# Optimization experiments

Measured on AMD Instinct MI355X. Metric: run time of the kernel, lower is better.

## Reference

```python
import jax, jax.numpy as jnp
import numpy as np

B, L, H, F, K, NBINS, T = 32, 512, 512, 512, 3, 256, 4096
EPS = 1e-8  # RMSNorm epsilon
PAD = (K - 1) // 2  # =1, matches both conv paddings in the torch module


def _conv1d(x, w, b):
    # x: [B, L, Cin], w: [K, Cin, Cout]
    return jax.lax.conv_general_dilated(
        x, w, window_strides=(1,), padding=[(PAD, PAD)],
        dimension_numbers=('NLC', 'LIO', 'NLC')) + b


def _rms(x, g):
    return g * x / (jnp.sqrt(jnp.mean(x * x, axis=-1, keepdims=True)) + EPS)


def _vpred(x, mask, w1, b1, g1, w2, b2, g2, wl, bl):
    h = _rms(jax.nn.relu(_conv1d(x, w1, b1)), g1)
    h = _rms(jax.nn.relu(_conv1d(h, w2, b2)), g2)
    out = (h @ wl + bl)[..., 0]  # [B, L]
    return jnp.where(mask, 0.0, out)


def _proj(x, w1, b1, w2, b2):
    return jax.nn.relu(jax.nn.relu(x @ w1 + b1) @ w2 + b2)


def _length_regulate(x, dur, max_len):
    # Vectorized equivalent of LengthRegulator: repeat phoneme i dur[b,i] times, pad to max_len.
    cum = jnp.cumsum(dur, axis=1)               # [B, L]
    mel_len = cum[:, -1]                        # [B]
    t = jnp.arange(max_len)                     # [T]
    idx = jax.vmap(lambda c: jnp.searchsorted(c, t, side='right'))(cum)  # [B, T]
    idx = jnp.minimum(idx, x.shape[1] - 1)
    out = jnp.take_along_axis(x, idx[:, :, None], axis=1)  # [B, T, H]
    valid = (t[None, :] < mel_len[:, None])
    return out * valid[:, :, None].astype(x.dtype), mel_len


def setup_inputs() -> dict:
    key = jax.random.key(0)
    ks = iter(jax.random.split(key, 64))
    n = lambda *s: jax.random.normal(next(ks), s, jnp.float32) * 0.05
    inp = {}
    inp['x'] = jax.random.normal(next(ks), (B, L, H), jnp.float32)
    inp['embedding'] = jax.random.normal(next(ks), (B, L, H), jnp.float32)
    inp['src_mask'] = jnp.zeros((B, L), bool)
    inp['duration_target'] = jax.random.randint(next(ks), (B, L), 0, 9, jnp.int32)
    inp['pitch_target'] = jax.random.normal(next(ks), (B, L), jnp.float32)
    inp['energy_target'] = jax.random.normal(next(ks), (B, L), jnp.float32)
    inp['max_len'] = T
    for p in ['dur', 'pit', 'eng']:
        inp[p + '_w1'] = n(K, H, F); inp[p + '_b1'] = jnp.zeros(F, jnp.float32)
        inp[p + '_g1'] = jnp.ones(F, jnp.float32)
        inp[p + '_w2'] = n(K, F, F); inp[p + '_b2'] = jnp.zeros(F, jnp.float32)
        inp[p + '_g2'] = jnp.ones(F, jnp.float32)
        inp[p + '_wl'] = n(F, 1); inp[p + '_bl'] = jnp.zeros(1, jnp.float32)
    for p in ['pp', 'ep', 'sp']:
        inp[p + '_w1'] = n(H, H); inp[p + '_b1'] = jnp.zeros(H, jnp.float32)
        inp[p + '_w2'] = n(H, H); inp[p + '_b2'] = jnp.zeros(H, jnp.float32)
    inp['pitch_bins'] = jnp.linspace(-3.0, 3.0, NBINS - 1)
    inp['energy_bins'] = jnp.linspace(-3.0, 3.0, NBINS - 1)
    inp['pitch_emb'] = n(NBINS, H)
    inp['energy_emb'] = n(NBINS, H)
    return inp


def reference(x, embedding, src_mask, duration_target, pitch_target, energy_target, max_len,
              dur_w1, dur_b1, dur_g1, dur_w2, dur_b2, dur_g2, dur_wl, dur_bl,
              pit_w1, pit_b1, pit_g1, pit_w2, pit_b2, pit_g2, pit_wl, pit_bl,
              eng_w1, eng_b1, eng_g1, eng_w2, eng_b2, eng_g2, eng_wl, eng_bl,
              pp_w1, pp_b1, pp_w2, pp_b2,
              ep_w1, ep_b1, ep_w2, ep_b2,
              sp_w1, sp_b1, sp_w2, sp_b2,
              pitch_bins, energy_bins, pitch_emb, energy_emb):
    log_dur = _vpred(x, src_mask, dur_w1, dur_b1, dur_g1, dur_w2, dur_b2, dur_g2, dur_wl, dur_bl)
    pit_pred = _vpred(x + _proj(embedding, pp_w1, pp_b1, pp_w2, pp_b2), src_mask,
                      pit_w1, pit_b1, pit_g1, pit_w2, pit_b2, pit_g2, pit_wl, pit_bl)
    pitch_embedding = pitch_emb[jnp.searchsorted(pitch_bins, pitch_target)]  # torch.bucketize right=False == side='left'
    eng_pred = _vpred(x + _proj(embedding, ep_w1, ep_b1, ep_w2, ep_b2), src_mask,
                      eng_w1, eng_b1, eng_g1, eng_w2, eng_b2, eng_g2, eng_wl, eng_bl)
    energy_embedding = energy_emb[jnp.searchsorted(energy_bins, energy_target)]
    xo = x + energy_embedding + pitch_embedding + _proj(embedding, sp_w1, sp_b1, sp_w2, sp_b2)
    out, mel_len = _length_regulate(xo, duration_target, max_len)
    return (out, pit_pred, eng_pred, log_dur, mel_len)
```

## Files before the change

kernel.cpp:

```cpp
#include <hip/hip_runtime.h>

#define Bv    32
#define Lv    512
#define Hv    512
#define Fv    512
#define Tv    4096
#define Mv    (Bv*Lv)
#define NBINSv 256

#define OUT_OFF 0
#define PIT_OFF (Bv*(size_t)Tv*Hv)
#define ENG_OFF (PIT_OFF + Mv)
#define DUR_OFF (ENG_OFF + Mv)
#define MEL_OFF (DUR_OFF + Mv)

typedef unsigned short ushort;
typedef __attribute__((ext_vector_type(8))) short   bf16x8;
typedef __attribute__((ext_vector_type(4))) float   f32x4;
typedef __attribute__((ext_vector_type(8))) unsigned short u16x8;

__device__ __forceinline__ float b2f(ushort u) {
    union { float f; unsigned u; } x; x.u = ((unsigned)u) << 16; return x.f;
}
__device__ __forceinline__ ushort f2b(float f) {
    union { float f; unsigned u; } x; x.f = f;
    unsigned r = x.u + 0x7fffu + ((x.u >> 16) & 1u);
    return (ushort)(r >> 16);
}

#define GLL16(g, l) __builtin_amdgcn_global_load_lds( \
    (const __attribute__((address_space(1))) void*)(g), \
    (__attribute__((address_space(3))) void*)(l), 16, 0, 0)

template<int NZ> struct GArgs {
    const ushort* A[NZ];
    const ushort* W[NZ];
    const float*  bias[NZ];
    ushort*       C[NZ];
};
struct RmsArgs   { const ushort* h[3]; const float* g[3]; ushort* o[3]; };
struct RlArgs    { const ushort* h[3]; const float* g[3]; const float* wl[3]; const float* bl[3]; };
struct TransArgs { const float* src[6]; ushort* dst[6]; };
struct ConvArgs  { const float* src[2]; ushort* dst[2]; };

template<int NTAPS, int EPI, int NZ>
__global__ __launch_bounds__(256) void gemm_bf16_kernel(
    GArgs<NZ> ga, const float* __restrict__ res, const float* __restrict__ pe,
    const float* __restrict__ ee, const int* __restrict__ idxp,
    const int* __restrict__ idxe, const ushort* __restrict__ zp)
{
    constexpr int KTOT = NTAPS * 512;
    const int z = (NZ > 1) ? blockIdx.z : 0;
    const ushort* __restrict__ A    = ga.A[z];
    const ushort* __restrict__ Bt   = ga.W[z];
    const float*  __restrict__ bias = ga.bias[z];
    ushort*       __restrict__ C    = ga.C[z];

    __shared__ ushort As[128 * 32];
    __shared__ ushort Bs[128 * 32];

    const int tid = threadIdx.x;
    const int n0 = blockIdx.x * 128;
    const int m0 = blockIdx.y * 128;

    const int sar = tid >> 2;
    const int sl  = tid & 3;

    const int lane = tid & 63;
    const int w    = tid >> 6;
    const int wm   = (w & 1) * 64;
    const int wn   = (w >> 1) * 64;
    const int lr   = lane & 15;
    const int q    = lane >> 4;

    f32x4 acc[4][4];
    #pragma unroll
    for (int i = 0; i < 4; ++i)
        #pragma unroll
        for (int j = 0; j < 4; ++j) {
            f32x4 zz = {0.f, 0.f, 0.f, 0.f};
            acc[i][j] = zz;
        }

    for (int kt = 0; kt < NTAPS * 16; ++kt) {
        const int tap = (NTAPS == 3) ? (kt >> 4) : 0;
        const int kin = (NTAPS == 3) ? ((kt & 15) << 5) : (kt << 5);

        #pragma unroll
        for (int r = 0; r < 2; ++r) {
            const int row = sar + r * 64;
            const int m   = m0 + row;
            const int qg  = (sl - (row >> 1)) & 3;
            const ushort* asrc;
            if (NTAPS == 3) {
                const int l  = m & (Lv - 1);
                const int ls = l + tap - 1;
                asrc = ((unsigned)ls < (unsigned)Lv)
                     ? A + (size_t)(m + tap - 1) * 512 + kin + qg * 8
                     : zp;
            } else {
                asrc = A + (size_t)m * 512 + kin + qg * 8;
            }
            GLL16(asrc, &As[row * 32 + sl * 8]);
            const ushort* bsrc = Bt + (size_t)(n0 + row) * KTOT + tap * 512 + kin + qg * 8;
            GLL16(bsrc, &Bs[row * 32 + sl * 8]);
        }
        __syncthreads();

        bf16x8 af[4], bfr[4];
        #pragma unroll
        for (int i = 0; i < 4; ++i) {
            const int rm = wm + i * 16 + lr;
            af[i]  = *(const bf16x8*)&As[rm * 32 + (((q + (rm >> 1)) & 3) << 3)];
            const int rn = wn + i * 16 + lr;
            bfr[i] = *(const bf16x8*)&Bs[rn * 32 + (((q + (rn >> 1)) & 3) << 3)];
        }
        #pragma unroll
        for (int i = 0; i < 4; ++i)
            #pragma unroll
            for (int j = 0; j < 4; ++j)
                acc[i][j] = __builtin_amdgcn_mfma_f32_16x16x32_bf16(
                                af[i], bfr[j], acc[i][j], 0, 0, 0);
        __syncthreads();
    }

    #pragma unroll
    for (int i = 0; i < 4; ++i) {
        #pragma unroll
        for (int r = 0; r < 4; ++r) {
            const int m = m0 + wm + i * 16 + q * 4 + r;
            const size_t ro = (size_t)m * 512;
            int ip = 0, ie = 0;
            if (EPI == 2) { ip = idxp[m]; ie = idxe[m]; }
            #pragma unroll
            for (int j = 0; j < 4; ++j) {
                const int n = n0 + wn + j * 16 + lr;
                float v = acc[i][j][r] + bias[n];
                v = fmaxf(v, 0.f);
                if (EPI >= 1) v += res[ro + n];
                if (EPI == 2) v += pe[(size_t)ip * 512 + n] + ee[(size_t)ie * 512 + n];
                C[ro + n] = f2b(v);
            }
        }
    }
}

__global__ __launch_bounds__(256) void convert_kernel(ConvArgs ca)
{
    const float* __restrict__ X  = ca.src[blockIdx.y];
    ushort*      __restrict__ Xb = ca.dst[blockIdx.y];
    const size_t i = (size_t)blockIdx.x * 256 + threadIdx.x;
    const float4 a = ((const float4*)X)[2 * i];
    const float4 b = ((const float4*)X)[2 * i + 1];
    u16x8 o;
    o[0] = f2b(a.x); o[1] = f2b(a.y); o[2] = f2b(a.z); o[3] = f2b(a.w);
    o[4] = f2b(b.x); o[5] = f2b(b.y); o[6] = f2b(b.z); o[7] = f2b(b.w);
    *(u16x8*)(Xb + i * 8) = o;
}

__global__ __launch_bounds__(256) void transpose_kernel(TransArgs ta, int Ktot)
{
    const float* __restrict__ W  = ta.src[blockIdx.z];
    ushort*      __restrict__ Wt = ta.dst[blockIdx.z];
    __shared__ float t[32][33];
    const int k0 = blockIdx.x * 32, n0 = blockIdx.y * 32;
    const int r = threadIdx.x >> 5, c = threadIdx.x & 31;
    #pragma unroll
    for (int rr = 0; rr < 4; ++rr)
        t[r + rr * 8][c] = W[(size_t)(k0 + r + rr * 8) * 512 + n0 + c];
    __syncthreads();
    #pragma unroll
    for (int rr = 0; rr < 4; ++rr)
        Wt[(size_t)(n0 + r + rr * 8) * Ktot + k0 + c] = f2b(t[c][r + rr * 8]);
}

__global__ __launch_bounds__(128) void rms_kernel(RmsArgs ra)
{
    const int z = blockIdx.y;
    const int row = blockIdx.x;
    const int tid = threadIdx.x;
    const ushort* __restrict__ h = ra.h[z];
    const ushort4 hv = ((const ushort4*)(h + (size_t)row * 512))[tid];
    const float v0 = b2f(hv.x), v1 = b2f(hv.y), v2 = b2f(hv.z), v3 = b2f(hv.w);
    float ss = v0 * v0 + v1 * v1 + v2 * v2 + v3 * v3;
    #pragma unroll
    for (int off = 32; off; off >>= 1) ss += __shfl_down(ss, off, 64);
    __shared__ float p[2];
    if ((tid & 63) == 0) p[tid >> 6] = ss;
    __syncthreads();
    const float tot = p[0] + p[1];
    const float inv = 1.f / (sqrtf(tot * (1.f / 512.f)) + 1e-8f);
    const float4 gv = ((const float4*)ra.g[z])[tid];
    ushort4 ov;
    ov.x = f2b(gv.x * v0 * inv); ov.y = f2b(gv.y * v1 * inv);
    ov.z = f2b(gv.z * v2 * inv); ov.w = f2b(gv.w * v3 * inv);
    ((ushort4*)(ra.o[z] + (size_t)row * 512))[tid] = ov;
}

__global__ __launch_bounds__(256) void rmslin_kernel(
    RlArgs ra, const unsigned char* __restrict__ mask, float* __restrict__ predbase)
{
    const int z = blockIdx.y;
    const int wave = threadIdx.x >> 6, lane = threadIdx.x & 63;
    const int row = blockIdx.x * 4 + wave;
    const ushort* __restrict__ h = ra.h[z];
    const bf16x8 hv = *(const bf16x8*)(h + (size_t)row * 512 + lane * 8);
    const float4 g0 = *(const float4*)(ra.g[z] + lane * 8);
    const float4 g1 = *(const float4*)(ra.g[z] + lane * 8 + 4);
    const float4 w0 = *(const float4*)(ra.wl[z] + lane * 8);
    const float4 w1 = *(const float4*)(ra.wl[z] + lane * 8 + 4);
    float hf[8];
    #pragma unroll
    for (int t = 0; t < 8; ++t) hf[t] = b2f((ushort)hv[t]);
    float ss = 0.f, sgw = 0.f;
    #pragma unroll
    for (int t = 0; t < 8; ++t) ss += hf[t] * hf[t];
    sgw += hf[0]*g0.x*w0.x + hf[1]*g0.y*w0.y + hf[2]*g0.z*w0.z + hf[3]*g0.w*w0.w;
    sgw += hf[4]*g1.x*w1.x + hf[5]*g1.y*w1.y + hf[6]*g1.z*w1.z + hf[7]*g1.w*w1.w;
    #pragma unroll
    for (int off = 32; off; off >>= 1) {
        ss  += __shfl_down(ss,  off, 64);
        sgw += __shfl_down(sgw, off, 64);
    }
    if (lane == 0) {
        const float inv = 1.f / (sqrtf(ss * (1.f / 512.f)) + 1e-8f);
        predbase[(size_t)z * Mv + row] = mask[row] ? 0.f : (sgw * inv + ra.bl[z][0]);
    }
}

__global__ __launch_bounds__(256) void idx_kernel(
    const float* __restrict__ pt, const float* __restrict__ et,
    const float* __restrict__ pbins, const float* __restrict__ ebins,
    int* __restrict__ idxp, int* __restrict__ idxe)
{
    __shared__ float pb[NBINSv - 1], ebn[NBINSv - 1];
    const int tid = threadIdx.x;
    if (tid < NBINSv - 1) { pb[tid] = pbins[tid]; ebn[tid] = ebins[tid]; }
    __syncthreads();
    const int m = blockIdx.x * 256 + tid;
    const float pv = pt[m], ev = et[m];
    int lo = 0, hi = NBINSv - 1;
    while (lo < hi) { int mid = (lo + hi) >> 1; if (pb[mid] < pv) lo = mid + 1; else hi = mid; }
    idxp[m] = lo;
    lo = 0; hi = NBINSv - 1;
    while (lo < hi) { int mid = (lo + hi) >> 1; if (ebn[mid] < ev) lo = mid + 1; else hi = mid; }
    idxe[m] = lo;
}

__global__ __launch_bounds__(512) void cumsum_kernel(
    const int* __restrict__ dur, int* __restrict__ cum,
    int* __restrict__ melint, float* __restrict__ melout)
{
    __shared__ int s[Lv];
    const int b = blockIdx.x, tid = threadIdx.x;
    s[tid] = dur[b * Lv + tid];
    __syncthreads();
    for (int off = 1; off < Lv; off <<= 1) {
        int t = (tid >= off) ? s[tid - off] : 0;
        __syncthreads();
        s[tid] += t;
        __syncthreads();
    }
    cum[b * Lv + tid] = s[tid];
    if (tid == Lv - 1) { melint[b] = s[tid]; melout[b] = (float)s[tid]; }
}

__global__ __launch_bounds__(256) void tmap_kernel(
    const int* __restrict__ cum, const int* __restrict__ melint,
    int* __restrict__ tmap)
{
    const int bt = blockIdx.x * 256 + threadIdx.x;
    const int b = bt >> 12;
    const int t = bt & (Tv - 1);
    const int* c = cum + b * Lv;
    int lo = 0, hi = Lv;
    while (lo < hi) { int mid = (lo + hi) >> 1; if (c[mid] <= t) lo = mid + 1; else hi = mid; }
    tmap[bt] = (t < melint[b]) ? (b * Lv + min(lo, Lv - 1)) : -1;
}

__global__ __launch_bounds__(128) void regulate_kernel(
    const ushort* __restrict__ xo, const int* __restrict__ tmap,
    float* __restrict__ out)
{
    const int bt = blockIdx.x;
    const int src = tmap[bt];
    float4 v = make_float4(0.f, 0.f, 0.f, 0.f);
    if (src >= 0) {
        const ushort4 u = ((const ushort4*)(xo + (size_t)src * 512))[threadIdx.x];
        v.x = b2f(u.x); v.y = b2f(u.y); v.z = b2f(u.z); v.w = b2f(u.w);
    }
    ((float4*)(out + (size_t)bt * 512))[threadIdx.x] = v;
}

extern "C" void kernel_launch(void* const* d_in, const int* in_sizes, int n_in,
                              void* d_out, int out_size, void* d_ws, size_t ws_size,
                              hipStream_t stream)
{
    const float* x    = (const float*)d_in[0];
    const float* emb  = (const float*)d_in[1];
    const unsigned char* mask = (const unsigned char*)d_in[2];
    const int*   durt = (const int*)d_in[3];
    const float* pt   = (const float*)d_in[4];
    const float* et   = (const float*)d_in[5];
    const float* dw1 = (const float*)d_in[7],  *db1 = (const float*)d_in[8],
               * dg1 = (const float*)d_in[9],  *dw2 = (const float*)d_in[10],
               * db2 = (const float*)d_in[11], *dg2 = (const float*)d_in[12],
               * dwl = (const float*)d_in[13], *dbl = (const float*)d_in[14];
    const float* pw1 = (const float*)d_in[15], *pb1 = (const float*)d_in[16],
               * pg1 = (const float*)d_in[17], *pw2 = (const float*)d_in[18],
               * pb2 = (const float*)d_in[19], *pg2 = (const float*)d_in[20],
               * pwl = (const float*)d_in[21], *pbl = (const float*)d_in[22];
    const float* ew1 = (const float*)d_in[23], *eb1 = (const float*)d_in[24],
               * eg1 = (const float*)d_in[25], *ew2 = (const float*)d_in[26],
               * eb2 = (const float*)d_in[27], *eg2 = (const float*)d_in[28],
               * ewl = (const float*)d_in[29], *ebl = (const float*)d_in[30];
    const float* ppw1 = (const float*)d_in[31], *ppb1 = (const float*)d_in[32],
               * ppw2 = (const float*)d_in[33], *ppb2 = (const float*)d_in[34];
    const float* epw1 = (const float*)d_in[35], *epb1 = (const float*)d_in[36],
               * epw2 = (const float*)d_in[37], *epb2 = (const float*)d_in[38];
    const float* spw1 = (const float*)d_in[39], *spb1 = (const float*)d_in[40],
               * spw2 = (const float*)d_in[41], *spb2 = (const float*)d_in[42];
    const float* pbins = (const float*)d_in[43];
    const float* ebins = (const float*)d_in[44];
    const float* pemb  = (const float*)d_in[45];
    const float* eemb  = (const float*)d_in[46];

    float* outf = (float*)d_out;

    int*    cum    = (int*)d_ws;
    int*    melint = cum + 16384;
    int*    idxp   = melint + 64;
    int*    idxe   = idxp + 16384;
    ushort* zp     = (ushort*)(idxe + 16384);
    int*    tmap   = idxe + 16448;
    ushort* xob    = (ushort*)((float*)d_ws + 262144);

    #define OBUF(i) ((ushort*)(outf + (size_t)(i) * 4194304))
    ushort* xb  = OBUF(0);   ushort* eb  = OBUF(1);
    ushort* pA0 = OBUF(2);   ushort* pA1 = OBUF(3);  ushort* pA2 = OBUF(4);
    ushort* xp  = OBUF(5);   ushort* xe  = OBUF(6);
    ushort* c0  = OBUF(7);   ushort* c1  = OBUF(8);  ushort* c2  = OBUF(9);
    ushort* r0  = OBUF(10);  ushort* r1  = OBUF(11); ushort* r2  = OBUF(12);
    ushort* wt[12];
    {
        size_t off = 13ull * 4194304;
        for (int i = 0; i < 6; ++i)  { wt[i] = (ushort*)(outf + off); off += 393216; }
        for (int i = 6; i < 12; ++i) { wt[i] = (ushort*)(outf + off); off += 131072; }
    }

    hipMemsetAsync(zp, 0, 64, stream);

    { ConvArgs ca = {{x, emb}, {xb, eb}};
      convert_kernel<<<dim3(4096, 2), 256, 0, stream>>>(ca); }
    { TransArgs ta = {{dw1, dw2, pw1, pw2, ew1, ew2}, {wt[0], wt[1], wt[2], wt[3], wt[4], wt[5]}};
      transpose_kernel<<<dim3(48, 16, 6), 256, 0, stream>>>(ta, 1536); }
    { TransArgs ta = {{ppw1, ppw2, epw1, epw2, spw1, spw2},
                      {wt[6], wt[7], wt[8], wt[9], wt[10], wt[11]}};
      transpose_kernel<<<dim3(16, 16, 6), 256, 0, stream>>>(ta, 512); }

    idx_kernel<<<Mv / 256, 256, 0, stream>>>(pt, et, pbins, ebins, idxp, idxe);
    cumsum_kernel<<<Bv, Lv, 0, stream>>>(durt, cum, melint, outf + MEL_OFF);
    tmap_kernel<<<Bv * Tv / 256, 256, 0, stream>>>(cum, melint, tmap);

    const dim3 g3(Fv / 128, Mv / 128, 3);
    const dim3 g2(Fv / 128, Mv / 128, 2);
    const dim3 g1(Fv / 128, Mv / 128, 1);

    { GArgs<3> a = {{eb, eb, eb}, {wt[6], wt[8], wt[10]}, {ppb1, epb1, spb1}, {pA0, pA1, pA2}};
      gemm_bf16_kernel<1, 0, 3><<<g3, 256, 0, stream>>>(a, nullptr, nullptr, nullptr,
                                                        nullptr, nullptr, zp); }
    { GArgs<2> a = {{pA0, pA1}, {wt[7], wt[9]}, {ppb2, epb2}, {xp, xe}};
      gemm_bf16_kernel<1, 1, 2><<<g2, 256, 0, stream>>>(a, x, nullptr, nullptr,
                                                        nullptr, nullptr, zp); }
    { GArgs<1> a = {{pA2}, {wt[11]}, {spb2}, {xob}};
      gemm_bf16_kernel<1, 2, 1><<<g1, 256, 0, stream>>>(a, x, pemb, eemb, idxp, idxe, zp); }

    { GArgs<3> a = {{xp, xe, xb}, {wt[2], wt[4], wt[0]}, {pb1, eb1, db1}, {c0, c1, c2}};
      gemm_bf16_kernel<3, 0, 3><<<g3, 256, 0, stream>>>(a, nullptr, nullptr, nullptr,
                                                        nullptr, nullptr, zp); }
    { RmsArgs ra = {{c0, c1, c2}, {pg1, eg1, dg1}, {r0, r1, r2}};
      rms_kernel<<<dim3(Mv, 3), 128, 0, stream>>>(ra); }
    { GArgs<3> a = {{r0, r1, r2}, {wt[3], wt[5], wt[1]}, {pb2, eb2, db2}, {c0, c1, c2}};
      gemm_bf16_kernel<3, 0, 3><<<g3, 256, 0, stream>>>(a, nullptr, nullptr, nullptr,
                                                        nullptr, nullptr, zp); }
    { RlArgs ra = {{c0, c1, c2}, {pg2, eg2, dg2}, {pwl, ewl, dwl}, {pbl, ebl, dbl}};
      rmslin_kernel<<<dim3(Mv / 4, 3), 256, 0, stream>>>(ra, mask, outf + PIT_OFF); }

    regulate_kernel<<<Bv * Tv, 128, 0, stream>>>(xob, tmap, outf + OUT_OFF);
}
```

Measured before the change: 845.0 us.

## Rewrite GEMM as 256x256 tile, 8-wave, double-buffered LDS pipeline

Replaces the 128x128, 4-wave, single-buffered GEMM with a 256x256 tile, 512-thread kernel. It uses a K-step of 64, double-buffered LDS, XOR swizzling, interleaved global-to-LDS prefetch with explicit vmcnt waits and barriers, and raised wave priority around MFMA bursts. The aim is to hide global load latency and raise MFMA utilisation by overlapping staging with compute and reusing data more per tile. The costs are 128KB of LDS per block and fewer blocks: the grid drops to 2x64xZ. That can leave CUs idle, and the hand-scheduled barrier and wait sequence is fragile.

Result: faster. 799.2 us (-5.4%).

```diff
diff --git a/kernel.cpp b/kernel.cpp
--- a/kernel.cpp
+++ b/kernel.cpp
@@ -31,6 +31,10 @@
 #define GLL16(g, l) __builtin_amdgcn_global_load_lds( \
     (const __attribute__((address_space(1))) void*)(g), \
     (__attribute__((address_space(3))) void*)(l), 16, 0, 0)
+
+#define FENCE() asm volatile("" ::: "memory")
+#define BAR() do { FENCE(); __builtin_amdgcn_s_barrier(); FENCE(); } while (0)
+#define VMCNT(N) asm volatile("s_waitcnt vmcnt(" #N ")" ::: "memory")
 
 template<int NZ> struct GArgs {
     const ushort* A[NZ];
@@ -43,98 +47,174 @@
 struct TransArgs { const float* src[6]; ushort* dst[6]; };
 struct ConvArgs  { const float* src[2]; ushort* dst[2]; };
 
+#define MFMA_Q(IOFF, JOFF)                                               \
+    do {                                                                 \
+        __builtin_amdgcn_s_setprio(1);                                   \
+        _Pragma("unroll")                                                \
+        for (int s_ = 0; s_ < 2; ++s_)                                   \
+            _Pragma("unroll")                                            \
+            for (int i_ = 0; i_ < 4; ++i_)                               \
+                _Pragma("unroll")                                        \
+                for (int j_ = 0; j_ < 2; ++j_)                           \
+                    acc[(IOFF) + i_][(JOFF) + j_] =                      \
+                        __builtin_amdgcn_mfma_f32_16x16x32_bf16(         \
+                            a_f[i_][s_], b_f[(JOFF) + j_][s_],           \
+                            acc[(IOFF) + i_][(JOFF) + j_], 0, 0, 0);     \
+        __builtin_amdgcn_s_setprio(0);                                   \
+    } while (0)
+
 template<int NTAPS, int EPI, int NZ>
-__global__ __launch_bounds__(256) void gemm_bf16_kernel(
+__global__ __launch_bounds__(512) void gemm256_kernel(
     GArgs<NZ> ga, const float* __restrict__ res, const float* __restrict__ pe,
     const float* __restrict__ ee, const int* __restrict__ idxp,
     const int* __restrict__ idxe, const ushort* __restrict__ zp)
 {
     constexpr int KTOT = NTAPS * 512;
+    constexpr int NT   = KTOT / 64;
     const int z = (NZ > 1) ? blockIdx.z : 0;
     const ushort* __restrict__ A    = ga.A[z];
     const ushort* __restrict__ Bt   = ga.W[z];
     const float*  __restrict__ bias = ga.bias[z];
     ushort*       __restrict__ C    = ga.C[z];
 
-    __shared__ ushort As[128 * 32];
-    __shared__ ushort Bs[128 * 32];
-
-    const int tid = threadIdx.x;
-    const int n0 = blockIdx.x * 128;
-    const int m0 = blockIdx.y * 128;
-
-    const int sar = tid >> 2;
-    const int sl  = tid & 3;
-
+    __shared__ ushort As[2][256][64];
+    __shared__ ushort Bs[2][256][64];
+
+    const int tid  = threadIdx.x;
+    const int n0   = blockIdx.x * 256;
+    const int m0   = blockIdx.y * 256;
     const int lane = tid & 63;
     const int w    = tid >> 6;
-    const int wm   = (w & 1) * 64;
-    const int wn   = (w >> 1) * 64;
+    const int wr   = w >> 2;
+    const int wc   = w & 3;
     const int lr   = lane & 15;
     const int q    = lane >> 4;
 
-    f32x4 acc[4][4];
-    #pragma unroll
-    for (int i = 0; i < 4; ++i)
+    const int srow = tid >> 3;
+    const int scol = ((tid & 7) ^ (srow & 7)) << 3;
+
+    auto stageA = [&](int buf, int h, int kt) {
+        const int tap = (NTAPS == 3) ? (kt >> 3) : 0;
+        const int kin = (NTAPS == 3) ? ((kt & 7) << 6) : (kt << 6);
+        #pragma unroll
+        for (int r = 0; r < 2; ++r) {
+            const int row = h * 128 + r * 64 + srow;
+            const int m   = m0 + row;
+            const ushort* src;
+            if (NTAPS == 3) {
+                const int ls = (m & (Lv - 1)) + tap - 1;
+                src = ((unsigned)ls < (unsigned)Lv)
+                    ? A + (size_t)(m + tap - 1) * 512 + kin + scol
+                    : zp;
+            } else {
+                src = A + (size_t)m * 512 + kin + scol;
+            }
+            GLL16(src, ((ushort*)As) + buf * 16384 + h * 8192 + r * 4096 + tid * 8);
+        }
+    };
+    auto stageB = [&](int buf, int h, int kt) {
+        #pragma unroll
+        for (int r = 0; r < 2; ++r) {
+            const int n = n0 + h * 128 + r * 64 + srow;
+            const ushort* src = Bt + (size_t)n * KTOT + kt * 64 + scol;
+            GLL16(src, ((ushort*)Bs) + buf * 16384 + h * 8192 + r * 4096 + tid * 8);
+        }
+    };
+
+    const int ca0 = ((q * 16) ^ ((lr & 7) << 4)) >> 1;
+    const int ca1 = (((64 + q * 16)) ^ ((lr & 7) << 4)) >> 1;
+    auto readA = [&](int buf, int i8, int s) -> bf16x8 {
+        const int rm = wr * 128 + i8 * 16 + lr;
+        return *(const bf16x8*)(((const ushort*)As) + buf * 16384 + rm * 64 + (s ? ca1 : ca0));
+    };
+    auto readB = [&](int buf, int j, int s) -> bf16x8 {
+        const int rn = wc * 64 + j * 16 + lr;
+        return *(const bf16x8*)(((const ushort*)Bs) + buf * 16384 + rn * 64 + (s ? ca1 : ca0));
+    };
+
+    f32x4 acc[8][4];
+    #pragma unroll
+    for (int i = 0; i < 8; ++i)
         #pragma unroll
         for (int j = 0; j < 4; ++j) {
             f32x4 zz = {0.f, 0.f, 0.f, 0.f};
             acc[i][j] = zz;
         }
-
-    for (int kt = 0; kt < NTAPS * 16; ++kt) {
-        const int tap = (NTAPS == 3) ? (kt >> 4) : 0;
-        const int kin = (NTAPS == 3) ? ((kt & 15) << 5) : (kt << 5);
-
-        #pragma unroll
-        for (int r = 0; r < 2; ++r) {
-            const int row = sar + r * 64;
-            const int m   = m0 + row;
-            const int qg  = (sl - (row >> 1)) & 3;
-            const ushort* asrc;
-            if (NTAPS == 3) {
-                const int l  = m & (Lv - 1);
-                const int ls = l + tap - 1;
-                asrc = ((unsigned)ls < (unsigned)Lv)
-                     ? A + (size_t)(m + tap - 1) * 512 + kin + qg * 8
-                     : zp;
-            } else {
-                asrc = A + (size_t)m * 512 + kin + qg * 8;
-            }
-            GLL16(asrc, &As[row * 32 + sl * 8]);
-            const ushort* bsrc = Bt + (size_t)(n0 + row) * KTOT + tap * 512 + kin + qg * 8;
-            GLL16(bsrc, &Bs[row * 32 + sl * 8]);
-        }
-        __syncthreads();
-
-        bf16x8 af[4], bfr[4];
-        #pragma unroll
-        for (int i = 0; i < 4; ++i) {
-            const int rm = wm + i * 16 + lr;
-            af[i]  = *(const bf16x8*)&As[rm * 32 + (((q + (rm >> 1)) & 3) << 3)];
-            const int rn = wn + i * 16 + lr;
-            bfr[i] = *(const bf16x8*)&Bs[rn * 32 + (((q + (rn >> 1)) & 3) << 3)];
-        }
-        #pragma unroll
-        for (int i = 0; i < 4; ++i)
-            #pragma unroll
-            for (int j = 0; j < 4; ++j)
-                acc[i][j] = __builtin_amdgcn_mfma_f32_16x16x32_bf16(
-                                af[i], bfr[j], acc[i][j], 0, 0, 0);
-        __syncthreads();
-    }
-
-    #pragma unroll
-    for (int i = 0; i < 4; ++i) {
+    bf16x8 a_f[4][2], b_f[4][2];
+
+    stageA(0, 0, 0); stageA(0, 1, 0);
+    stageB(0, 0, 0); stageB(0, 1, 0);
+    stageA(1, 0, 1);
+    stageB(1, 0, 1); stageB(1, 1, 1);
+    VMCNT(6);
+    BAR();
+
+    #pragma unroll 1
+    for (int t = 0; t < NT; t += 2) {
+        const bool pf = (t + 2 < NT);
+        #pragma unroll
+        for (int i = 0; i < 4; ++i) { a_f[i][0] = readA(0, i, 0); a_f[i][1] = readA(0, i, 1); }
+        #pragma unroll
+        for (int j = 0; j < 2; ++j) { b_f[j][0] = readB(0, j, 0); b_f[j][1] = readB(0, j, 1); }
+        stageA(1, 1, t + 1);
+        BAR();
+        MFMA_Q(0, 0);
+        BAR();
+        #pragma unroll
+        for (int j = 2; j < 4; ++j) { b_f[j][0] = readB(0, j, 0); b_f[j][1] = readB(0, j, 1); }
+        if (pf) stageA(0, 0, t + 2);
+        BAR();
+        MFMA_Q(0, 2);
+        BAR();
+        #pragma unroll
+        for (int i = 0; i < 4; ++i) { a_f[i][0] = readA(0, 4 + i, 0); a_f[i][1] = readA(0, 4 + i, 1); }
+        if (pf) stageB(0, 0, t + 2);
+        BAR();
+        MFMA_Q(4, 0);
+        BAR();
+        if (pf) { stageB(0, 1, t + 2); VMCNT(6); }
+        else    { VMCNT(0); }
+        BAR();
+        MFMA_Q(4, 2);
+        BAR();
+        #pragma unroll
+        for (int i = 0; i < 4; ++i) { a_f[i][0] = readA(1, i, 0); a_f[i][1] = readA(1, i, 1); }
+        #pragma unroll
+        for (int j = 0; j < 2; ++j) { b_f[j][0] = readB(1, j, 0); b_f[j][1] = readB(1, j, 1); }
+        if (pf) stageA(0, 1, t + 2);
+        BAR();
+        MFMA_Q(0, 0);
+        BAR();
+        #pragma unroll
+        for (int j = 2; j < 4; ++j) { b_f[j][0] = readB(1, j, 0); b_f[j][1] = readB(1, j, 1); }
+        if (pf) stageA(1, 0, t + 3);
+        BAR();
+        MFMA_Q(0, 2);
+        BAR();
+        #pragma unroll
+        for (int i = 0; i < 4; ++i) { a_f[i][0] = readA(1, 4 + i, 0); a_f[i][1] = readA(1, 4 + i, 1); }
+        if (pf) stageB(1, 0, t + 3);
+        BAR();
+        MFMA_Q(4, 0);
+        BAR();
+        if (pf) stageB(1, 1, t + 3);
+        VMCNT(6);
+        BAR();
+        MFMA_Q(4, 2);
+        BAR();
+    }
+
+    #pragma unroll
+    for (int i = 0; i < 8; ++i) {
         #pragma unroll
         for (int r = 0; r < 4; ++r) {
-            const int m = m0 + wm + i * 16 + q * 4 + r;
+            const int m = m0 + wr * 128 + i * 16 + q * 4 + r;
             const size_t ro = (size_t)m * 512;
             int ip = 0, ie = 0;
             if (EPI == 2) { ip = idxp[m]; ie = idxe[m]; }
             #pragma unroll
             for (int j = 0; j < 4; ++j) {
-                const int n = n0 + wn + j * 16 + lr;
+                const int n = n0 + wc * 64 + j * 16 + lr;
                 float v = acc[i][j][r] + bias[n];
                 v = fmaxf(v, 0.f);
                 if (EPI >= 1) v += res[ro + n];
@@ -362,27 +442,27 @@
     cumsum_kernel<<<Bv, Lv, 0, stream>>>(durt, cum, melint, outf + MEL_OFF);
     tmap_kernel<<<Bv * Tv / 256, 256, 0, stream>>>(cum, melint, tmap);
 
-    const dim3 g3(Fv / 128, Mv / 128, 3);
-    const dim3 g2(Fv / 128, Mv / 128, 2);
-    const dim3 g1(Fv / 128, Mv / 128, 1);
+    const dim3 g3(Fv / 256, Mv / 256, 3);
+    const dim3 g2(Fv / 256, Mv / 256, 2);
+    const dim3 g1(Fv / 256, Mv / 256, 1);
 
     { GArgs<3> a = {{eb, eb, eb}, {wt[6], wt[8], wt[10]}, {ppb1, epb1, spb1}, {pA0, pA1, pA2}};
-      gemm_bf16_kernel<1, 0, 3><<<g3, 256, 0, stream>>>(a, nullptr, nullptr, nullptr,
-                                                        nullptr, nullptr, zp); }
+      gemm256_kernel<1, 0, 3><<<g3, 512, 0, stream>>>(a, nullptr, nullptr, nullptr,
+                                                      nullptr, nullptr, zp); }
     { GArgs<2> a = {{pA0, pA1}, {wt[7], wt[9]}, {ppb2, epb2}, {xp, xe}};
-      gemm_bf16_kernel<1, 1, 2><<<g2, 256, 0, stream>>>(a, x, nullptr, nullptr,
-                                                        nullptr, nullptr, zp); }
+      gemm256_kernel<1, 1, 2><<<g2, 512, 0, stream>>>(a, x, nullptr, nullptr,
+                                                      nullptr, nullptr, zp); }
     { GArgs<1> a = {{pA2}, {wt[11]}, {spb2}, {xob}};
-      gemm_bf16_kernel<1, 2, 1><<<g1, 256, 0, stream>>>(a, x, pemb, eemb, idxp, idxe, zp); }
+      gemm256_kernel<1, 2, 1><<<g1, 512, 0, stream>>>(a, x, pemb, eemb, idxp, idxe, zp); }
 
     { GArgs<3> a = {{xp, xe, xb}, {wt[2], wt[4], wt[0]}, {pb1, eb1, db1}, {c0, c1, c2}};
-      gemm_bf16_kernel<3, 0, 3><<<g3, 256, 0, stream>>>(a, nullptr, nullptr, nullptr,
-                                                        nullptr, nullptr, zp); }
+      gemm256_kernel<3, 0, 3><<<g3, 512, 0, stream>>>(a, nullptr, nullptr, nullptr,
+                                                      nullptr, nullptr, zp); }
     { RmsArgs ra = {{c0, c1, c2}, {pg1, eg1, dg1}, {r0, r1, r2}};
       rms_kernel<<<dim3(Mv, 3), 128, 0, stream>>>(ra); }
     { GArgs<3> a = {{r0, r1, r2}, {wt[3], wt[5], wt[1]}, {pb2, eb2, db2}, {c0, c1, c2}};
-      gemm_bf16_kernel<3, 0, 3><<<g3, 256, 0, stream>>>(a, nullptr, nullptr, nullptr,
-                                                        nullptr, nullptr, zp); }
+      gemm256_kernel<3, 0, 3><<<g3, 512, 0, stream>>>(a, nullptr, nullptr, nullptr,
+                                                      nullptr, nullptr, zp); }
     { RlArgs ra = {{c0, c1, c2}, {pg2, eg2, dg2}, {pwl, ewl, dwl}, {pbl, ebl, dbl}};
       rmslin_kernel<<<dim3(Mv / 4, 3), 256, 0, stream>>>(ra, mask, outf + PIT_OFF); }
 
```

## Merge projection second-layer GEMMs into one launch and swizzle blocks across XCDs

Applied to the files above, without the earlier changes.

Combines the two second-layer projection GEMM launches (pitch/energy with residual, and the speaker one with embedding adds) into a single z=3 launch. The epilogue mode is selected per z at runtime. All GEMMs also remap the linear block id so that consecutive tiles land on the same XCD, improving L2 reuse of A/W tiles. The cost is a small runtime branch in the epilogue and an index remap that assumes the workgroup count divides by 8.

Measured after the change: 822.3 us. 2.7% less time.

```diff
diff --git a/kernel.cpp b/kernel.cpp
--- a/kernel.cpp
+++ b/kernel.cpp
@@ -50,7 +50,16 @@
     const int* __restrict__ idxe, const ushort* __restrict__ zp)
 {
     constexpr int KTOT = NTAPS * 512;
-    const int z = (NZ > 1) ? blockIdx.z : 0;
+    constexpr int GX   = Fv / 128;
+    constexpr int GY   = Mv / 128;
+    constexpr int NWG  = GX * GY * NZ;
+
+    int lin = blockIdx.x + GX * (blockIdx.y + GY * blockIdx.z);
+    lin = (lin & 7) * (NWG >> 3) + (lin >> 3);
+    const int bx = lin & (GX - 1);
+    const int by = (lin >> 2) & (GY - 1);
+    const int z  = (NZ > 1) ? (lin / (GX * GY)) : 0;
+
     const ushort* __restrict__ A    = ga.A[z];
     const ushort* __restrict__ Bt   = ga.W[z];
     const float*  __restrict__ bias = ga.bias[z];
@@ -60,8 +69,8 @@
     __shared__ ushort Bs[128 * 32];
 
     const int tid = threadIdx.x;
-    const int n0 = blockIdx.x * 128;
-    const int m0 = blockIdx.y * 128;
+    const int n0 = bx * 128;
+    const int m0 = by * 128;
 
     const int sar = tid >> 2;
     const int sl  = tid & 3;
@@ -124,6 +133,8 @@
         __syncthreads();
     }
 
+    int epi = EPI;
+    if (EPI == 3) epi = (z == 2) ? 2 : 1;
     #pragma unroll
     for (int i = 0; i < 4; ++i) {
         #pragma unroll
@@ -131,14 +142,14 @@
             const int m = m0 + wm + i * 16 + q * 4 + r;
             const size_t ro = (size_t)m * 512;
             int ip = 0, ie = 0;
-            if (EPI == 2) { ip = idxp[m]; ie = idxe[m]; }
+            if (EPI >= 2 && epi == 2) { ip = idxp[m]; ie = idxe[m]; }
             #pragma unroll
             for (int j = 0; j < 4; ++j) {
                 const int n = n0 + wn + j * 16 + lr;
                 float v = acc[i][j][r] + bias[n];
                 v = fmaxf(v, 0.f);
-                if (EPI >= 1) v += res[ro + n];
-                if (EPI == 2) v += pe[(size_t)ip * 512 + n] + ee[(size_t)ie * 512 + n];
+                if (EPI != 0 && epi >= 1) v += res[ro + n];
+                if (EPI >= 2 && epi == 2) v += pe[(size_t)ip * 512 + n] + ee[(size_t)ie * 512 + n];
                 C[ro + n] = f2b(v);
             }
         }
@@ -363,17 +374,13 @@
     tmap_kernel<<<Bv * Tv / 256, 256, 0, stream>>>(cum, melint, tmap);
 
     const dim3 g3(Fv / 128, Mv / 128, 3);
-    const dim3 g2(Fv / 128, Mv / 128, 2);
-    const dim3 g1(Fv / 128, Mv / 128, 1);
 
     { GArgs<3> a = {{eb, eb, eb}, {wt[6], wt[8], wt[10]}, {ppb1, epb1, spb1}, {pA0, pA1, pA2}};
       gemm_bf16_kernel<1, 0, 3><<<g3, 256, 0, stream>>>(a, nullptr, nullptr, nullptr,
                                                         nullptr, nullptr, zp); }
-    { GArgs<2> a = {{pA0, pA1}, {wt[7], wt[9]}, {ppb2, epb2}, {xp, xe}};
-      gemm_bf16_kernel<1, 1, 2><<<g2, 256, 0, stream>>>(a, x, nullptr, nullptr,
-                                                        nullptr, nullptr, zp); }
-    { GArgs<1> a = {{pA2}, {wt[11]}, {spb2}, {xob}};
-      gemm_bf16_kernel<1, 2, 1><<<g1, 256, 0, stream>>>(a, x, pemb, eemb, idxp, idxe, zp); }
+    { GArgs<3> a = {{pA0, pA1, pA2}, {wt[7], wt[9], wt[11]}, {ppb2, epb2, spb2}, {xp, xe, xob}};
+      gemm_bf16_kernel<1, 3, 3><<<g3, 256, 0, stream>>>(a, x, pemb, eemb,
+                                                        idxp, idxe, zp); }
 
     { GArgs<3> a = {{xp, xe, xb}, {wt[2], wt[4], wt[0]}, {pb1, eb1, db1}, {c0, c1, c2}};
       gemm_bf16_kernel<3, 0, 3><<<g3, 256, 0, stream>>>(a, nullptr, nullptr, nullptr,
```
